# Kernel optimization log

Measured on AMD Instinct MI355X. Metric: run time of the kernel, lower is better.

## Reference

```python
import jax, jax.numpy as jnp
import numpy as np
from jax import lax

B, T, U_LEN, FEAT = 4, 128, 64, 80
H = 1024        # encoder_size == pred_net_size
VOCAB = 64
EMB = 64
JOINT = 640
SMAX = 4096


def setup_inputs() -> dict:
    key = jax.random.key(0)
    ks = jax.random.split(key, 24)
    s = 0.02

    def n(k, shape):
        return jax.random.normal(k, shape, jnp.float32) * s

    inp = {}
    inp["encoder_inp"] = jax.random.normal(ks[0], (B, T, FEAT), jnp.float32)
    inp["pred_inp"] = jax.random.randint(ks[1], (B, U_LEN), 0, VOCAB)
    inp["encoder_state"] = jnp.zeros((2, B, H), jnp.float32)
    # encoder LSTM layers (keras gate order i,f,c,o packed in last dim)
    inp["enc_W0"] = n(ks[2], (FEAT, 4 * H)); inp["enc_U0"] = n(ks[3], (H, 4 * H)); inp["enc_b0"] = jnp.zeros((4 * H,), jnp.float32)
    inp["enc_W1"] = n(ks[4], (H, 4 * H));    inp["enc_U1"] = n(ks[5], (H, 4 * H)); inp["enc_b1"] = jnp.zeros((4 * H,), jnp.float32)
    # prediction network
    inp["embed"] = n(ks[6], (VOCAB, EMB))
    inp["pred_W0"] = n(ks[7], (EMB, 4 * H)); inp["pred_U0"] = n(ks[8], (H, 4 * H)); inp["pred_b0"] = jnp.zeros((4 * H,), jnp.float32)
    inp["pred_W1"] = n(ks[9], (H, 4 * H));   inp["pred_U1"] = n(ks[10], (H, 4 * H)); inp["pred_b1"] = jnp.zeros((4 * H,), jnp.float32)
    # joint network + softmax dense + projection
    inp["Wj"] = n(ks[11], (H, JOINT));    inp["bj"] = jnp.zeros((JOINT,), jnp.float32)
    inp["Ws"] = n(ks[12], (JOINT, SMAX)); inp["bs"] = jnp.zeros((SMAX,), jnp.float32)
    inp["Wp"] = n(ks[13], (SMAX, VOCAB)); inp["bp"] = jnp.zeros((VOCAB,), jnp.float32)
    return inp


def _lstm(x, h0, c0, W, Uw, b):
    """Keras-style LSTM, return_sequences + final (h, c). x: [B,T,F]."""
    xg = jnp.einsum('btf,fg->btg', x, W) + b  # precompute input projection

    def step(carry, xt):
        h, c = carry
        g = xt + h @ Uw
        i, f, gg, o = jnp.split(g, 4, axis=-1)
        c = jax.nn.sigmoid(f) * c + jax.nn.sigmoid(i) * jnp.tanh(gg)
        h = jax.nn.sigmoid(o) * jnp.tanh(c)
        return (h, c), h

    (h, c), hs = lax.scan(step, (h0, c0), jnp.swapaxes(xg, 0, 1))
    return jnp.swapaxes(hs, 0, 1), h, c


def reference(encoder_inp, pred_inp, encoder_state,
              enc_W0, enc_U0, enc_b0, enc_W1, enc_U1, enc_b1,
              embed, pred_W0, pred_U0, pred_b0, pred_W1, pred_U1, pred_b1,
              Wj, bj, Ws, bs, Wp, bp):
    h0, c0 = encoder_state[0], encoder_state[1]
    # encoder: every layer is initialized with the same incoming state (as in source)
    x, sh, sc = _lstm(encoder_inp, h0, c0, enc_W0, enc_U0, enc_b0)
    x, sh, sc = _lstm(x, h0, c0, enc_W1, enc_U1, enc_b1)
    new_enc_state = jnp.stack([sh, sc])  # [2,B,H]

    # prediction network (zero initial state, keras default)
    z = jnp.zeros_like(h0)
    p = embed[pred_inp]  # [B,U,EMB]
    p, _, _ = _lstm(p, z, z, pred_W0, pred_U0, pred_b0)
    p, _, _ = _lstm(p, z, z, pred_W1, pred_U1, pred_b1)

    # joint: broadcast-add [B,T,U,H] -> Dense -> softmax Dense -> projection
    j = x[:, :, None, :] + p[:, None, :, :]
    jd = j @ Wj + bj                                 # [B,T,U,JOINT]
    s = jax.nn.softmax(jd @ Ws + bs, axis=-1)        # [B,T,U,SMAX]
    out = s @ Wp + bp                                # [B,T,U,VOCAB]
    return out, new_enc_state
```

## Files before the change

### kernel.cpp

```cpp
#include <hip/hip_runtime.h>
#include <stdint.h>

typedef unsigned short ushort_t;

#define HD 1024
#define G4 4096
#define NB 4
#define TT 128
#define UU 64
#define NFEAT 80
#define SMAXD 4096
#define JD 640
#define NV 64

static __device__ __forceinline__ float lo2f(uint32_t u) {
  union { uint32_t i; float f; } v; v.i = u << 16; return v.f;
}
static __device__ __forceinline__ float hi2f(uint32_t u) {
  union { uint32_t i; float f; } v; v.i = u & 0xffff0000u; return v.f;
}
static __device__ __forceinline__ ushort_t f2bf(float f) {
  union { uint32_t i; float f; } v; v.f = f;
  return (ushort_t)((v.i + 0x7fffu + ((v.i >> 16) & 1u)) >> 16);
}

__global__ void transpose_f32(const float* __restrict__ src, float* __restrict__ dst,
                              int K, int N) {
  __shared__ float tile[32][33];
  int n0 = blockIdx.x * 32, k0 = blockIdx.y * 32;
  int tx = threadIdx.x, ty = threadIdx.y;
#pragma unroll
  for (int j = 0; j < 32; j += 8)
    tile[ty + j][tx] = src[(size_t)(k0 + ty + j) * N + n0 + tx];
  __syncthreads();
#pragma unroll
  for (int j = 0; j < 32; j += 8)
    dst[(size_t)(n0 + ty + j) * K + k0 + tx] = tile[tx][ty + j];
}

__global__ void transpose_bf16(const float* __restrict__ src, ushort_t* __restrict__ dst,
                               int K, int N) {
  __shared__ float tile[32][33];
  int n0 = blockIdx.x * 32, k0 = blockIdx.y * 32;
  int tx = threadIdx.x, ty = threadIdx.y;
#pragma unroll
  for (int j = 0; j < 32; j += 8)
    tile[ty + j][tx] = src[(size_t)(k0 + ty + j) * N + n0 + tx];
  __syncthreads();
#pragma unroll
  for (int j = 0; j < 32; j += 8)
    dst[(size_t)(n0 + ty + j) * K + k0 + tx] = f2bf(tile[tx][ty + j]);
}

__global__ __launch_bounds__(256) void inproj_kernel(
    const float* __restrict__ X, const float* __restrict__ W,
    const float* __restrict__ bias, float* __restrict__ C, int K) {
  __shared__ float xls[JD];
  int m = blockIdx.x;
  int tid = threadIdx.x;
  for (int i = tid; i < K; i += 256) xls[i] = X[(size_t)m * K + i];
  __syncthreads();
  for (int c = tid; c < G4; c += 256) {
    float acc = bias[c];
    for (int k = 0; k < K; ++k) acc = fmaf(xls[k], W[(size_t)k * G4 + c], acc);
    C[(size_t)m * G4 + c] = acc;
  }
}

__global__ __launch_bounds__(256) void cs_kernel(const float* __restrict__ bj,
                                                 const float* __restrict__ Ws,
                                                 const float* __restrict__ bs,
                                                 float* __restrict__ cs) {
  __shared__ float bl[JD];
  int tid = threadIdx.x;
  for (int i = tid; i < JD; i += 256) bl[i] = bj[i];
  __syncthreads();
  int c = blockIdx.x * 256 + tid;
  float acc = bs[c];
  for (int k = 0; k < JD; ++k) acc = fmaf(bl[k], Ws[(size_t)k * G4 + c], acc);
  cs[c] = acc;
}

__global__ __launch_bounds__(256) void gemm_kernel(
    const float* __restrict__ A, const float* __restrict__ Bm,
    const float* __restrict__ bias, float* __restrict__ C,
    int M, int N, int K) {
  __shared__ float As[32][68];
  __shared__ float Bs[32][68];
  int n0 = blockIdx.x * 64, m0 = blockIdx.y * 64;
  int tid = threadIdx.x;
  int tx = tid & 15, ty = tid >> 4;
  float acc[4][4] = {};
  for (int k0 = 0; k0 < K; k0 += 32) {
#pragma unroll
    for (int i = 0; i < 8; ++i) {
      int idx = tid + i * 256;
      int ml = idx >> 5, kl = idx & 31;
      As[kl][ml] = A[(size_t)(m0 + ml) * K + k0 + kl];
      int kl2 = idx >> 6, nl = idx & 63;
      Bs[kl2][nl] = Bm[(size_t)(k0 + kl2) * N + n0 + nl];
    }
    __syncthreads();
#pragma unroll 8
    for (int k = 0; k < 32; ++k) {
      float4 a4 = *(const float4*)&As[k][ty * 4];
      float4 b4 = *(const float4*)&Bs[k][tx * 4];
      acc[0][0] = fmaf(a4.x, b4.x, acc[0][0]);
      acc[0][1] = fmaf(a4.x, b4.y, acc[0][1]);
      acc[0][2] = fmaf(a4.x, b4.z, acc[0][2]);
      acc[0][3] = fmaf(a4.x, b4.w, acc[0][3]);
      acc[1][0] = fmaf(a4.y, b4.x, acc[1][0]);
      acc[1][1] = fmaf(a4.y, b4.y, acc[1][1]);
      acc[1][2] = fmaf(a4.y, b4.z, acc[1][2]);
      acc[1][3] = fmaf(a4.y, b4.w, acc[1][3]);
      acc[2][0] = fmaf(a4.z, b4.x, acc[2][0]);
      acc[2][1] = fmaf(a4.z, b4.y, acc[2][1]);
      acc[2][2] = fmaf(a4.z, b4.z, acc[2][2]);
      acc[2][3] = fmaf(a4.z, b4.w, acc[2][3]);
      acc[3][0] = fmaf(a4.w, b4.x, acc[3][0]);
      acc[3][1] = fmaf(a4.w, b4.y, acc[3][1]);
      acc[3][2] = fmaf(a4.w, b4.z, acc[3][2]);
      acc[3][3] = fmaf(a4.w, b4.w, acc[3][3]);
    }
    __syncthreads();
  }
  float b0 = 0.f, b1 = 0.f, b2 = 0.f, b3 = 0.f;
  if (bias) {
    b0 = bias[n0 + tx * 4 + 0]; b1 = bias[n0 + tx * 4 + 1];
    b2 = bias[n0 + tx * 4 + 2]; b3 = bias[n0 + tx * 4 + 3];
  }
#pragma unroll
  for (int i = 0; i < 4; ++i) {
    float4 o;
    o.x = acc[i][0] + b0; o.y = acc[i][1] + b1; o.z = acc[i][2] + b2; o.w = acc[i][3] + b3;
    *(float4*)&C[(size_t)(m0 + ty * 4 + i) * N + n0 + tx * 4] = o;
  }
}

__global__ __launch_bounds__(256, 1) void lstm_kernel(
    const float* __restrict__ xgA, int lenA,
    const float* __restrict__ UtA,
    const float* __restrict__ cinitA,
    float* __restrict__ hseqA,
    float* __restrict__ hbufA,
    float* __restrict__ finalA,
    const float* __restrict__ xgB, int lenB,
    const int* __restrict__ tokB,
    const ushort_t* __restrict__ UtB,
    float* __restrict__ hseqB,
    float* __restrict__ hbufB,
    unsigned int* __restrict__ flagsA,
    unsigned int* __restrict__ flagsB) {
  __shared__ float hprev[NB][HD];
  __shared__ float red[8][NB][32];
  __shared__ float gl[NB][32];
  __shared__ float cst[NB][8];
  int blk = blockIdx.x;
  int isA = (blk < 128) ? 1 : 0;
  int p = blk & 127;
  int tid = threadIdx.x;
  int c = tid & 31, s = tid >> 5;
  int len = isA ? lenA : lenB;
  const float* xg = isA ? xgA : xgB;
  float* hseq = isA ? hseqA : hseqB;
  float* hbuf = isA ? hbufA : hbufB;
  unsigned int* flags = isA ? flagsA : flagsB;

  if (tid < 32) {
    int bb = tid >> 3, hh = tid & 7;
    cst[bb][hh] = (isA && cinitA) ? cinitA[bb * HD + p * 8 + hh] : 0.0f;
  }

  int gate = c >> 3, hic = c & 7;
  int ucol = gate * HD + p * 8 + hic;
  int kb = s * 128;

  float u[128];
  if (isA) {
    const float4* ur = (const float4*)(UtA + (size_t)ucol * HD + kb);
#pragma unroll
    for (int i = 0; i < 32; ++i) ((float4*)u)[i] = ur[i];
  } else {
    const uint4* ur = (const uint4*)(UtB + (size_t)ucol * HD + kb);
#pragma unroll
    for (int i = 0; i < 16; ++i) {
      uint4 q = ur[i];
      u[i * 8 + 0] = lo2f(q.x); u[i * 8 + 1] = hi2f(q.x);
      u[i * 8 + 2] = lo2f(q.y); u[i * 8 + 3] = hi2f(q.y);
      u[i * 8 + 4] = lo2f(q.z); u[i * 8 + 5] = hi2f(q.z);
      u[i * 8 + 6] = lo2f(q.w); u[i * 8 + 7] = hi2f(q.w);
    }
  }

  for (int t = 0; t < len; ++t) {
    int par = t & 1;
    const float* hsrc = hbuf + par * (NB * HD);
    {
      const float* pb = hsrc + tid * 16;
      float4 r0, r1, r2, r3;
      asm volatile(
          "global_load_dwordx4 %0, %4, off sc0 sc1\n\t"
          "global_load_dwordx4 %1, %4, off offset:16 sc0 sc1\n\t"
          "global_load_dwordx4 %2, %4, off offset:32 sc0 sc1\n\t"
          "global_load_dwordx4 %3, %4, off offset:48 sc0 sc1\n\t"
          "s_waitcnt vmcnt(0)"
          : "=&v"(r0), "=&v"(r1), "=&v"(r2), "=&v"(r3)
          : "v"(pb)
          : "memory");
      float4* hp4 = (float4*)&hprev[0][0];
      hp4[tid * 4 + 0] = r0;
      hp4[tid * 4 + 1] = r1;
      hp4[tid * 4 + 2] = r2;
      hp4[tid * 4 + 3] = r3;
    }
    __syncthreads();

    float aa[4] = {0.f, 0.f, 0.f, 0.f};
#pragma unroll
    for (int k4 = 0; k4 < 32; ++k4) {
#pragma unroll
      for (int bb = 0; bb < 4; ++bb) {
        float4 h4 = *(const float4*)&hprev[bb][kb + k4 * 4];
        aa[bb] = fmaf(u[k4 * 4 + 0], h4.x, aa[bb]);
        aa[bb] = fmaf(u[k4 * 4 + 1], h4.y, aa[bb]);
        aa[bb] = fmaf(u[k4 * 4 + 2], h4.z, aa[bb]);
        aa[bb] = fmaf(u[k4 * 4 + 3], h4.w, aa[bb]);
      }
    }
    red[s][0][c] = aa[0]; red[s][1][c] = aa[1];
    red[s][2][c] = aa[2]; red[s][3][c] = aa[3];
    __syncthreads();

    if (tid < 128) {
      int bb = tid >> 5, cc = tid & 31;
      float g = red[0][bb][cc] + red[1][bb][cc] + red[2][bb][cc] + red[3][bb][cc] +
                red[4][bb][cc] + red[5][bb][cc] + red[6][bb][cc] + red[7][bb][cc];
      int gg = cc >> 3, hh = cc & 7;
      int uc = gg * HD + p * 8 + hh;
      float xv;
      if (!isA && tokB) {
        int token = tokB[bb * lenB + t];
        xv = xg[(size_t)token * G4 + uc];
      } else {
        xv = xg[((size_t)bb * len + t) * G4 + uc];
      }
      gl[bb][cc] = g + xv;
    }
    __syncthreads();

    if (tid < 32) {
      int bb = tid >> 3, hh = tid & 7;
      float gi = gl[bb][hh], gf = gl[bb][8 + hh], gc = gl[bb][16 + hh], go = gl[bb][24 + hh];
      float si = 1.0f / (1.0f + expf(-gi));
      float sf = 1.0f / (1.0f + expf(-gf));
      float so = 1.0f / (1.0f + expf(-go));
      float cN = sf * cst[bb][hh] + si * tanhf(gc);
      float hN = so * tanhf(cN);
      cst[bb][hh] = cN;
      int hidx = p * 8 + hh;
      __hip_atomic_store(&hbuf[(par ^ 1) * (NB * HD) + bb * HD + hidx], hN,
                         __ATOMIC_RELAXED, __HIP_MEMORY_SCOPE_AGENT);
      hseq[((size_t)bb * len + t) * HD + hidx] = hN;
      if (isA && finalA && t == len - 1) {
        finalA[bb * HD + hidx] = hN;
        finalA[NB * HD + bb * HD + hidx] = cN;
      }
    }
    __syncthreads();

    if (t + 1 < len) {
      asm volatile("s_waitcnt vmcnt(0)" ::: "memory");
      if (tid == 0)
        __hip_atomic_store(&flags[p * 32], (unsigned)(t + 1),
                           __ATOMIC_RELAXED, __HIP_MEMORY_SCOPE_AGENT);
      if (tid < 128) {
        while (__hip_atomic_load(&flags[tid * 32], __ATOMIC_RELAXED,
                                 __HIP_MEMORY_SCOPE_AGENT) < (unsigned)(t + 1)) {
          __builtin_amdgcn_s_sleep(4);
        }
      }
      __syncthreads();
    }
  }
}

__global__ __launch_bounds__(256) void final_kernel(
    const float* __restrict__ xsA, const float* __restrict__ psA,
    const float* __restrict__ csA, const float* __restrict__ Wp,
    const float* __restrict__ bp, float* __restrict__ out) {
  __shared__ float xc[SMAXD];
  __shared__ float el[64][68];
  __shared__ float wl[64][68];
  __shared__ float Dl[64];
  int bt = blockIdx.x;
  int b = bt >> 7, t = bt & 127;
  int tid = threadIdx.x;
  int tx = tid & 15, uy = tid >> 4;
  for (int i = tid; i < SMAXD; i += 256) xc[i] = xsA[(size_t)bt * SMAXD + i] + csA[i];
  const float* psrow = psA + (size_t)b * UU * SMAXD;
  float acc[4][4] = {};
  float d0 = 0.f, d1 = 0.f, d2 = 0.f, d3 = 0.f;
  for (int k0 = 0; k0 < SMAXD; k0 += 64) {
    __syncthreads();
#pragma unroll
    for (int i = 0; i < 16; ++i) {
      int idx = tid + i * 256;
      int kl = idx >> 6, vl = idx & 63;
      wl[kl][vl] = Wp[(size_t)(k0 + kl) * NV + vl];
    }
#pragma unroll
    for (int i = 0; i < 16; ++i) {
      int idx = tid + i * 256;
      int u = idx >> 6, kl = idx & 63;
      float l = xc[k0 + kl] + psrow[(size_t)u * SMAXD + k0 + kl];
      el[kl][u] = __expf(l);
    }
    __syncthreads();
#pragma unroll 4
    for (int k = 0; k < 64; ++k) {
      float4 e4 = *(const float4*)&el[k][uy * 4];
      float4 w4 = *(const float4*)&wl[k][tx * 4];
      d0 += e4.x; d1 += e4.y; d2 += e4.z; d3 += e4.w;
      acc[0][0] = fmaf(e4.x, w4.x, acc[0][0]);
      acc[0][1] = fmaf(e4.x, w4.y, acc[0][1]);
      acc[0][2] = fmaf(e4.x, w4.z, acc[0][2]);
      acc[0][3] = fmaf(e4.x, w4.w, acc[0][3]);
      acc[1][0] = fmaf(e4.y, w4.x, acc[1][0]);
      acc[1][1] = fmaf(e4.y, w4.y, acc[1][1]);
      acc[1][2] = fmaf(e4.y, w4.z, acc[1][2]);
      acc[1][3] = fmaf(e4.y, w4.w, acc[1][3]);
      acc[2][0] = fmaf(e4.z, w4.x, acc[2][0]);
      acc[2][1] = fmaf(e4.z, w4.y, acc[2][1]);
      acc[2][2] = fmaf(e4.z, w4.z, acc[2][2]);
      acc[2][3] = fmaf(e4.z, w4.w, acc[2][3]);
      acc[3][0] = fmaf(e4.w, w4.x, acc[3][0]);
      acc[3][1] = fmaf(e4.w, w4.y, acc[3][1]);
      acc[3][2] = fmaf(e4.w, w4.z, acc[3][2]);
      acc[3][3] = fmaf(e4.w, w4.w, acc[3][3]);
    }
  }
  if (tx == 0) {
    Dl[uy * 4 + 0] = d0; Dl[uy * 4 + 1] = d1;
    Dl[uy * 4 + 2] = d2; Dl[uy * 4 + 3] = d3;
  }
  __syncthreads();
#pragma unroll
  for (int j = 0; j < 4; ++j) {
    int u = uy * 4 + j;
    float dinv = 1.0f / Dl[u];
    float4 o;
    o.x = fmaf(acc[j][0], dinv, bp[tx * 4 + 0]);
    o.y = fmaf(acc[j][1], dinv, bp[tx * 4 + 1]);
    o.z = fmaf(acc[j][2], dinv, bp[tx * 4 + 2]);
    o.w = fmaf(acc[j][3], dinv, bp[tx * 4 + 3]);
    *(float4*)&out[(((size_t)(b * TT + t) * UU + u) * NV) + tx * 4] = o;
  }
}

extern "C" void kernel_launch(void* const* d_in, const int* in_sizes, int n_in,
                              void* d_out, int out_size, void* d_ws, size_t ws_size,
                              hipStream_t stream) {
  (void)in_sizes; (void)n_in; (void)out_size; (void)ws_size;
  const float* encoder_inp   = (const float*)d_in[0];
  const int*   pred_inp      = (const int*)d_in[1];
  const float* encoder_state = (const float*)d_in[2];
  const float* enc_W0 = (const float*)d_in[3];
  const float* enc_U0 = (const float*)d_in[4];
  const float* enc_b0 = (const float*)d_in[5];
  const float* enc_W1 = (const float*)d_in[6];
  const float* enc_U1 = (const float*)d_in[7];
  const float* enc_b1 = (const float*)d_in[8];
  const float* embed   = (const float*)d_in[9];
  const float* pred_W0 = (const float*)d_in[10];
  const float* pred_U0 = (const float*)d_in[11];
  const float* pred_b0 = (const float*)d_in[12];
  const float* pred_W1 = (const float*)d_in[13];
  const float* pred_U1 = (const float*)d_in[14];
  const float* pred_b1 = (const float*)d_in[15];
  const float* Wj = (const float*)d_in[16];
  const float* bj = (const float*)d_in[17];
  const float* Ws = (const float*)d_in[18];
  const float* bs = (const float*)d_in[19];
  const float* Wp = (const float*)d_in[20];
  const float* bp = (const float*)d_in[21];
  float* outp = (float*)d_out;

  char* wsb = (char*)d_ws;
  size_t off = 0;
  auto alloc = [&](size_t bytes) -> void* {
    void* p = (void*)(wsb + off);
    off += (bytes + 255) & ~(size_t)255;
    return p;
  };
  float*    Ut_e0 = (float*)alloc((size_t)G4 * HD * 4);
  float*    Ut_e1 = (float*)alloc((size_t)G4 * HD * 4);
  ushort_t* Ut_p0 = (ushort_t*)alloc((size_t)G4 * HD * 2);
  ushort_t* Ut_p1 = (ushort_t*)alloc((size_t)G4 * HD * 2);
  float* xg_e0 = (float*)alloc((size_t)NB * TT * G4 * 4);
  float* ptab  = (float*)alloc((size_t)NV * G4 * 4);
  float* xg_e1 = (float*)alloc((size_t)NB * TT * G4 * 4);
  float* xg_p1 = (float*)alloc((size_t)NB * UU * G4 * 4);
  float* h0s  = (float*)alloc((size_t)NB * TT * HD * 4);
  float* hp0s = (float*)alloc((size_t)NB * UU * HD * 4);
  float* h1s  = (float*)alloc((size_t)NB * TT * HD * 4);
  float* hp1s = (float*)alloc((size_t)NB * UU * HD * 4);
  float* xjb = (float*)alloc((size_t)NB * TT * JD * 4);
  float* pjb = (float*)alloc((size_t)NB * UU * JD * 4);
  float* xsb = (float*)alloc((size_t)NB * TT * SMAXD * 4);
  float* psb = (float*)alloc((size_t)NB * UU * SMAXD * 4);
  float* csb = (float*)alloc((size_t)SMAXD * 4);
  float* hbufs = (float*)alloc((size_t)4 * 2 * NB * HD * 4);
  unsigned int* bars = (unsigned int*)alloc((size_t)4 * 128 * 32 * 4);

  float* hbufA_enc  = hbufs;
  float* hbufA_pred = hbufs + 2 * NB * HD;
  float* hbufC_enc  = hbufs + 4 * NB * HD;
  float* hbufC_pred = hbufs + 6 * NB * HD;

  unsigned int* flags_e0 = bars;
  unsigned int* flags_p0 = bars + 1 * 128 * 32;
  unsigned int* flags_e1 = bars + 2 * 128 * 32;
  unsigned int* flags_p1 = bars + 3 * 128 * 32;

  hipMemsetAsync(hbufs, 0, (size_t)4 * 2 * NB * HD * 4, stream);
  hipMemsetAsync(bars, 0, (size_t)4 * 128 * 32 * 4, stream);
  hipMemcpyAsync(hbufA_enc, encoder_state, (size_t)NB * HD * 4, hipMemcpyDeviceToDevice, stream);
  hipMemcpyAsync(hbufC_enc, encoder_state, (size_t)NB * HD * 4, hipMemcpyDeviceToDevice, stream);

  dim3 tb(32, 8);
  transpose_f32 <<<dim3(G4 / 32, HD / 32), tb, 0, stream>>>(enc_U0, Ut_e0, HD, G4);
  transpose_f32 <<<dim3(G4 / 32, HD / 32), tb, 0, stream>>>(enc_U1, Ut_e1, HD, G4);
  transpose_bf16<<<dim3(G4 / 32, HD / 32), tb, 0, stream>>>(pred_U0, Ut_p0, HD, G4);
  transpose_bf16<<<dim3(G4 / 32, HD / 32), tb, 0, stream>>>(pred_U1, Ut_p1, HD, G4);

  inproj_kernel<<<NB * TT, 256, 0, stream>>>(encoder_inp, enc_W0, enc_b0, xg_e0, NFEAT);
  inproj_kernel<<<NV, 256, 0, stream>>>(embed, pred_W0, pred_b0, ptab, 64);

  lstm_kernel<<<256, 256, 0, stream>>>(
      xg_e0, TT, Ut_e0, encoder_state + NB * HD, h0s, hbufA_enc, nullptr,
      ptab, UU, pred_inp, Ut_p0, hp0s, hbufA_pred, flags_e0, flags_p0);

  gemm_kernel<<<dim3(G4 / 64, (NB * TT) / 64), 256, 0, stream>>>(h0s, enc_W1, enc_b1, xg_e1, NB * TT, G4, HD);
  gemm_kernel<<<dim3(G4 / 64, (NB * UU) / 64), 256, 0, stream>>>(hp0s, pred_W1, pred_b1, xg_p1, NB * UU, G4, HD);

  lstm_kernel<<<256, 256, 0, stream>>>(
      xg_e1, TT, Ut_e1, encoder_state + NB * HD, h1s, hbufC_enc,
      outp + (size_t)NB * TT * UU * NV,
      xg_p1, UU, nullptr, Ut_p1, hp1s, hbufC_pred, flags_e1, flags_p1);

  gemm_kernel<<<dim3(JD / 64, (NB * TT) / 64), 256, 0, stream>>>(h1s, Wj, nullptr, xjb, NB * TT, JD, HD);
  gemm_kernel<<<dim3(JD / 64, (NB * UU) / 64), 256, 0, stream>>>(hp1s, Wj, nullptr, pjb, NB * UU, JD, HD);
  gemm_kernel<<<dim3(SMAXD / 64, (NB * TT) / 64), 256, 0, stream>>>(xjb, Ws, nullptr, xsb, NB * TT, SMAXD, JD);
  gemm_kernel<<<dim3(SMAXD / 64, (NB * UU) / 64), 256, 0, stream>>>(pjb, Ws, nullptr, psb, NB * UU, SMAXD, JD);
  cs_kernel<<<SMAXD / 256, 256, 0, stream>>>(bj, Ws, bs, csb);

  final_kernel<<<NB * TT, 256, 0, stream>>>(xsb, psb, csb, Wp, bp, outp);
}
```

Before: 2.820 ms.

## Replace global flag barrier with per-chunk tagged hidden-state exchange in LSTM

The persistent LSTM kernel previously published hidden state to a flat buffer and then ran a full grid barrier (all 128 blocks spinning on each other's flags) every timestep. Now each block writes its 32 hidden values into its own 64-float chunk that carries a step tag, and consumers poll each chunk's tag before loading it. This removes the separate barrier round-trip and merges data and flag into one cache line. It relies on the relaxed-ordering tag write becoming visible after the data stores, which the s_waitcnt is meant to guarantee, and it adds per-thread spinning on 128 tags.

```diff
diff --git a/kernel.cpp b/kernel.cpp
--- a/kernel.cpp
+++ b/kernel.cpp
@@ -12,6 +12,7 @@
 #define SMAXD 4096
 #define JD 640
 #define NV 64
+#define CHK 64
 
 static __device__ __forceinline__ float lo2f(uint32_t u) {
   union { uint32_t i; float f; } v; v.i = u << 16; return v.f;
@@ -50,6 +51,17 @@
 #pragma unroll
   for (int j = 0; j < 32; j += 8)
     dst[(size_t)(n0 + ty + j) * K + k0 + tx] = f2bf(tile[tx][ty + j]);
+}
+
+__global__ void init_chunks(const float* __restrict__ state_h,
+                            float* __restrict__ chunksE0,
+                            float* __restrict__ chunksE1) {
+  int idx = blockIdx.x * 256 + threadIdx.x;
+  int bb = idx >> 10, rem = idx & 1023;
+  int p = rem >> 3, hh = rem & 7;
+  float v = state_h[idx];
+  chunksE0[p * CHK + bb * 8 + hh] = v;
+  chunksE1[p * CHK + bb * 8 + hh] = v;
 }
 
 __global__ __launch_bounds__(256) void inproj_kernel(
@@ -142,15 +154,13 @@
     const float* __restrict__ UtA,
     const float* __restrict__ cinitA,
     float* __restrict__ hseqA,
-    float* __restrict__ hbufA,
+    float* __restrict__ chunksA,
     float* __restrict__ finalA,
     const float* __restrict__ xgB, int lenB,
     const int* __restrict__ tokB,
     const ushort_t* __restrict__ UtB,
     float* __restrict__ hseqB,
-    float* __restrict__ hbufB,
-    unsigned int* __restrict__ flagsA,
-    unsigned int* __restrict__ flagsB) {
+    float* __restrict__ chunksB) {
   __shared__ float hprev[NB][HD];
   __shared__ float red[8][NB][32];
   __shared__ float gl[NB][32];
@@ -163,8 +173,7 @@
   int len = isA ? lenA : lenB;
   const float* xg = isA ? xgA : xgB;
   float* hseq = isA ? hseqA : hseqB;
-  float* hbuf = isA ? hbufA : hbufB;
-  unsigned int* flags = isA ? flagsA : flagsB;
+  float* chunks = isA ? chunksA : chunksB;
 
   if (tid < 32) {
     int bb = tid >> 3, hh = tid & 7;
@@ -192,11 +201,18 @@
     }
   }
 
+  int pp = tid >> 1, half = tid & 1;
+
   for (int t = 0; t < len; ++t) {
     int par = t & 1;
-    const float* hsrc = hbuf + par * (NB * HD);
     {
-      const float* pb = hsrc + tid * 16;
+      const float* chunk = chunks + (size_t)par * (128 * CHK) + pp * CHK;
+      const unsigned int* tagp = (const unsigned int*)(chunk + 32);
+      while ((int)__hip_atomic_load(tagp, __ATOMIC_RELAXED,
+                                    __HIP_MEMORY_SCOPE_AGENT) < t) {
+        __builtin_amdgcn_s_sleep(1);
+      }
+      const float* pb = chunk + half * 16;
       float4 r0, r1, r2, r3;
       asm volatile(
           "global_load_dwordx4 %0, %4, off sc0 sc1\n\t"
@@ -207,11 +223,11 @@
           : "=&v"(r0), "=&v"(r1), "=&v"(r2), "=&v"(r3)
           : "v"(pb)
           : "memory");
-      float4* hp4 = (float4*)&hprev[0][0];
-      hp4[tid * 4 + 0] = r0;
-      hp4[tid * 4 + 1] = r1;
-      hp4[tid * 4 + 2] = r2;
-      hp4[tid * 4 + 3] = r3;
+      int bb0 = half * 2;
+      float4* d0 = (float4*)&hprev[bb0][pp * 8];
+      d0[0] = r0; d0[1] = r1;
+      float4* d1 = (float4*)&hprev[bb0 + 1][pp * 8];
+      d1[0] = r2; d1[1] = r3;
     }
     __syncthreads();
 
@@ -258,29 +274,22 @@
       float hN = so * tanhf(cN);
       cst[bb][hh] = cN;
       int hidx = p * 8 + hh;
-      __hip_atomic_store(&hbuf[(par ^ 1) * (NB * HD) + bb * HD + hidx], hN,
+      float* chunkN = chunks + (size_t)(par ^ 1) * (128 * CHK) + p * CHK;
+      __hip_atomic_store(&chunkN[bb * 8 + hh], hN,
                          __ATOMIC_RELAXED, __HIP_MEMORY_SCOPE_AGENT);
       hseq[((size_t)bb * len + t) * HD + hidx] = hN;
       if (isA && finalA && t == len - 1) {
         finalA[bb * HD + hidx] = hN;
         finalA[NB * HD + bb * HD + hidx] = cN;
       }
-    }
-    __syncthreads();
-
-    if (t + 1 < len) {
       asm volatile("s_waitcnt vmcnt(0)" ::: "memory");
-      if (tid == 0)
-        __hip_atomic_store(&flags[p * 32], (unsigned)(t + 1),
+      if (tid == 0) {
+        unsigned int* tagN = (unsigned int*)(chunkN + 32);
+        __hip_atomic_store(tagN, (unsigned)(t + 1),
                            __ATOMIC_RELAXED, __HIP_MEMORY_SCOPE_AGENT);
-      if (tid < 128) {
-        while (__hip_atomic_load(&flags[tid * 32], __ATOMIC_RELAXED,
-                                 __HIP_MEMORY_SCOPE_AGENT) < (unsigned)(t + 1)) {
-          __builtin_amdgcn_s_sleep(4);
-        }
       }
-      __syncthreads();
-    }
+    }
+    __syncthreads();
   }
 }
 
@@ -409,23 +418,15 @@
   float* xsb = (float*)alloc((size_t)NB * TT * SMAXD * 4);
   float* psb = (float*)alloc((size_t)NB * UU * SMAXD * 4);
   float* csb = (float*)alloc((size_t)SMAXD * 4);
-  float* hbufs = (float*)alloc((size_t)4 * 2 * NB * HD * 4);
-  unsigned int* bars = (unsigned int*)alloc((size_t)4 * 128 * 32 * 4);
-
-  float* hbufA_enc  = hbufs;
-  float* hbufA_pred = hbufs + 2 * NB * HD;
-  float* hbufC_enc  = hbufs + 4 * NB * HD;
-  float* hbufC_pred = hbufs + 6 * NB * HD;
-
-  unsigned int* flags_e0 = bars;
-  unsigned int* flags_p0 = bars + 1 * 128 * 32;
-  unsigned int* flags_e1 = bars + 2 * 128 * 32;
-  unsigned int* flags_p1 = bars + 3 * 128 * 32;
-
-  hipMemsetAsync(hbufs, 0, (size_t)4 * 2 * NB * HD * 4, stream);
-  hipMemsetAsync(bars, 0, (size_t)4 * 128 * 32 * 4, stream);
-  hipMemcpyAsync(hbufA_enc, encoder_state, (size_t)NB * HD * 4, hipMemcpyDeviceToDevice, stream);
-  hipMemcpyAsync(hbufC_enc, encoder_state, (size_t)NB * HD * 4, hipMemcpyDeviceToDevice, stream);
+  float* chunks = (float*)alloc((size_t)4 * 2 * 128 * CHK * 4);
+
+  float* chk_e0 = chunks + 0 * (2 * 128 * CHK);
+  float* chk_p0 = chunks + 1 * (2 * 128 * CHK);
+  float* chk_e1 = chunks + 2 * (2 * 128 * CHK);
+  float* chk_p1 = chunks + 3 * (2 * 128 * CHK);
+
+  hipMemsetAsync(chunks, 0, (size_t)4 * 2 * 128 * CHK * 4, stream);
+  init_chunks<<<16, 256, 0, stream>>>(encoder_state, chk_e0, chk_e1);
 
   dim3 tb(32, 8);
   transpose_f32 <<<dim3(G4 / 32, HD / 32), tb, 0, stream>>>(enc_U0, Ut_e0, HD, G4);
@@ -437,16 +438,16 @@
   inproj_kernel<<<NV, 256, 0, stream>>>(embed, pred_W0, pred_b0, ptab, 64);
 
   lstm_kernel<<<256, 256, 0, stream>>>(
-      xg_e0, TT, Ut_e0, encoder_state + NB * HD, h0s, hbufA_enc, nullptr,
-      ptab, UU, pred_inp, Ut_p0, hp0s, hbufA_pred, flags_e0, flags_p0);
+      xg_e0, TT, Ut_e0, encoder_state + NB * HD, h0s, chk_e0, nullptr,
+      ptab, UU, pred_inp, Ut_p0, hp0s, chk_p0);
 
   gemm_kernel<<<dim3(G4 / 64, (NB * TT) / 64), 256, 0, stream>>>(h0s, enc_W1, enc_b1, xg_e1, NB * TT, G4, HD);
   gemm_kernel<<<dim3(G4 / 64, (NB * UU) / 64), 256, 0, stream>>>(hp0s, pred_W1, pred_b1, xg_p1, NB * UU, G4, HD);
 
   lstm_kernel<<<256, 256, 0, stream>>>(
-      xg_e1, TT, Ut_e1, encoder_state + NB * HD, h1s, hbufC_enc,
+      xg_e1, TT, Ut_e1, encoder_state + NB * HD, h1s, chk_e1,
       outp + (size_t)NB * TT * UU * NV,
-      xg_p1, UU, nullptr, Ut_p1, hp1s, hbufC_pred, flags_e1, flags_p1);
+      xg_p1, UU, nullptr, Ut_p1, hp1s, chk_p1);
 
   gemm_kernel<<<dim3(JD / 64, (NB * TT) / 64), 256, 0, stream>>>(h1s, Wj, nullptr, xjb, NB * TT, JD, HD);
   gemm_kernel<<<dim3(JD / 64, (NB * UU) / 64), 256, 0, stream>>>(hp1s, Wj, nullptr, pjb, NB * UU, JD, HD);
```

Result: no change. 2.808 ms (-0.5%).
